# Kernel optimization log

Hardware: AMD Instinct MI355X
Metric: run time of the kernel (lower is better)

Reference implementation:

```python
import jax, jax.numpy as jnp
import numpy as np

NUM_ENTITIES = 100000
NUM_RELATIONS = 500
DIM = 256
NUM_TRIANGLES = 300000
NUM_TETRAS = 150000
ET_EDGES = 900000   # ~3 entities per triangle
TT_EDGES = 600000   # ~4 triangles per tetra
ENT_TET_EDGES = 600000
BATCH = 8192


def _mean_aggregate(src_idx, dst_idx, src, num_dst):
    """Scatter-mean of src[src_idx] into num_dst buckets keyed by dst_idx."""
    agg = jax.ops.segment_sum(src[src_idx], dst_idx, num_segments=num_dst)
    cnt = jax.ops.segment_sum(jnp.ones_like(dst_idx, dtype=src.dtype), dst_idx,
                              num_segments=num_dst)
    return agg / jnp.maximum(cnt, 1.0)[:, None]


def setup_inputs() -> dict:
    key = jax.random.key(0)
    ks = jax.random.split(key, 16)
    s = 1.0 / np.sqrt(DIM)
    E = jax.random.normal(ks[0], (NUM_ENTITIES, DIM), jnp.float32) * s
    R = jax.random.normal(ks[1], (NUM_RELATIONS, DIM), jnp.float32) * s
    lin2_w = jax.random.normal(ks[2], (DIM, DIM), jnp.float32) * s
    lin2_b = jnp.zeros((DIM,), jnp.float32)
    lin3_w = jax.random.normal(ks[3], (DIM, DIM), jnp.float32) * s
    lin3_b = jnp.zeros((DIM,), jnp.float32)
    t2e_w = jax.random.normal(ks[4], (DIM, DIM), jnp.float32) * s
    t2e_b = jnp.zeros((DIM,), jnp.float32)
    fusion_alpha = jnp.zeros((2,), jnp.float32)
    gamma = jnp.array([12.0], jnp.float32)
    # bipartite edge lists: row 0 = src indices, row 1 = dst indices
    et = jnp.stack([
        jax.random.randint(ks[5], (ET_EDGES,), 0, NUM_ENTITIES),
        jax.random.randint(ks[6], (ET_EDGES,), 0, NUM_TRIANGLES)], axis=0)
    tt = jnp.stack([
        jax.random.randint(ks[7], (TT_EDGES,), 0, NUM_TRIANGLES),
        jax.random.randint(ks[8], (TT_EDGES,), 0, NUM_TETRAS)], axis=0)
    # entity_tetra_index: row 0 = entity, row 1 = tetra (flipped inside model)
    etet = jnp.stack([
        jax.random.randint(ks[9], (ENT_TET_EDGES,), 0, NUM_ENTITIES),
        jax.random.randint(ks[10], (ENT_TET_EDGES,), 0, NUM_TETRAS)], axis=0)
    triples = jnp.stack([
        jax.random.randint(ks[11], (BATCH,), 0, NUM_ENTITIES),
        jax.random.randint(ks[12], (BATCH,), 0, NUM_RELATIONS),
        jax.random.randint(ks[13], (BATCH,), 0, NUM_ENTITIES)], axis=1)
    return {"E": E, "R": R, "lin2_w": lin2_w, "lin2_b": lin2_b,
            "lin3_w": lin3_w, "lin3_b": lin3_b, "t2e_w": t2e_w, "t2e_b": t2e_b,
            "fusion_alpha": fusion_alpha, "gamma": gamma,
            "entity_triangle_index": et, "triangle_tetra_index": tt,
            "entity_tetra_index": etet, "triples": triples,
            "num_triangles": NUM_TRIANGLES, "num_tetras": NUM_TETRAS}


def reference(E, R, lin2_w, lin2_b, lin3_w, lin3_b, t2e_w, t2e_b,
              fusion_alpha, gamma, entity_triangle_index, triangle_tetra_index,
              entity_tetra_index, triples, num_triangles, num_tetras):
    # gnn2: entity -> triangle (scatter-mean + Linear + ReLU)
    tri_agg = _mean_aggregate(entity_triangle_index[0], entity_triangle_index[1],
                              E, num_triangles)                      # [T, d]
    tri_emb = jax.nn.relu(tri_agg @ lin2_w.T + lin2_b)
    # gnn3: triangle -> tetra
    tet_agg = _mean_aggregate(triangle_tetra_index[0], triangle_tetra_index[1],
                              tri_emb, num_tetras)                   # [K, d]
    tet_emb = jax.nn.relu(tet_agg @ lin3_w.T + lin3_b)
    tet_proj = tet_emb @ t2e_w.T + t2e_b                             # [K, d]
    # tetra -> entity (edge index flipped: src=tetra, dst=entity)
    v_topo = _mean_aggregate(entity_tetra_index[1], entity_tetra_index[0],
                             tet_proj, E.shape[0])                   # [N, d]
    # learned fusion
    w = jax.nn.softmax(fusion_alpha)
    V = w[0] * E + w[1] * v_topo
    # TransE scoring: gamma - ||V[h] + R[r] - V[t]||
    h, r, t = triples[:, 0], triples[:, 1], triples[:, 2]
    diff = V[h] + R[r] - V[t]
    return gamma[0] - jnp.sqrt(jnp.sum(diff * diff, axis=-1))
```

## Files before the change

### kernel.cpp

```cpp
#include <hip/hip_runtime.h>
#include <hip/hip_bf16.h>
#include <math.h>

#define DIM 256
#define SBS 256
#define SIT 16
#define NT   300000
#define NTET 150000

typedef __attribute__((ext_vector_type(8))) short          bf16x8;
typedef __attribute__((ext_vector_type(8))) unsigned short u16x8;
typedef __attribute__((ext_vector_type(4))) float          f32x4;

__device__ inline float b2f(unsigned short u) {
    union { unsigned int i; float f; } c; c.i = ((unsigned int)u) << 16; return c.f;
}
__device__ inline unsigned short f2b(float f) {
    __hip_bfloat16 h = __float2bfloat16(f);
    return *reinterpret_cast<unsigned short*>(&h);
}
__device__ inline short f2bs(float f) { return (short)f2b(f); }
__device__ inline bool bmget(const unsigned* bm, int i) {
    return (bm[i >> 5] >> (i & 31)) & 1u;
}
__device__ inline void gll16(const void* g, void* l) {
    __builtin_amdgcn_global_load_lds(
        (const __attribute__((address_space(1))) unsigned int*)g,
        (__attribute__((address_space(3))) unsigned int*)l, 16, 0, 0);
}

__global__ __launch_bounds__(256) void k_cast3(
    const float* __restrict__ w2, const float* __restrict__ w3,
    const float* __restrict__ wt, unsigned short* __restrict__ out)
{
    int i = (blockIdx.x * 256 + threadIdx.x) * 4;
    const float* src; int l;
    if (i < 65536)       { src = w2; l = i; }
    else if (i < 131072) { src = w3; l = i - 65536; }
    else                 { src = wt; l = i - 131072; }
    float4 v = *(const float4*)(src + l);
    ushort4 o; o.x = f2b(v.x); o.y = f2b(v.y); o.z = f2b(v.z); o.w = f2b(v.w);
    *(ushort4*)(out + i) = o;
}

__global__ __launch_bounds__(256) void k_mark(
    const int* __restrict__ trip, unsigned* __restrict__ bm, int B)
{
    int i = blockIdx.x * 256 + threadIdx.x;
    if (i < 2 * B) {
        int ent = trip[(i >> 1) * 3 + ((i & 1) ? 2 : 0)];
        atomicOr(&bm[ent >> 5], 1u << (ent & 31));
    }
}

__global__ __launch_bounds__(256) void k_markf(
    const int* __restrict__ mi, const int* __restrict__ ci,
    const unsigned* __restrict__ bmIn, unsigned* __restrict__ bmOut, int n)
{
    int e = blockIdx.x * 256 + threadIdx.x;
    if (e < n && bmget(bmIn, ci[e])) {
        int m = mi[e];
        unsigned msk = 1u << (m & 31);
        if (!(bmOut[m >> 5] & msk)) atomicOr(&bmOut[m >> 5], msk);
    }
}

__global__ __launch_bounds__(256) void k_bits(
    const unsigned* __restrict__ bm, int* __restrict__ out, int n)
{
    int i = blockIdx.x * 256 + threadIdx.x;
    if (i < n) out[i] = (bm[i >> 5] >> (i & 31)) & 1u;
}

__global__ __launch_bounds__(256) void k_count_all(
    const int* __restrict__ et, const int* __restrict__ tt, const int* __restrict__ etet,
    const unsigned* __restrict__ bmTri, const unsigned* __restrict__ bmTet,
    const unsigned* __restrict__ bmEnt, int* __restrict__ cnt,
    int ET, int TT, int ETET)
{
    int e = blockIdx.x * 256 + threadIdx.x;
    if (e < ET) {
        int d = et[ET + e];
        if (bmget(bmTri, d)) atomicAdd(&cnt[d], 1);
    } else if (e < ET + TT) {
        int i = e - ET;
        int d = tt[TT + i];
        if (bmget(bmTet, d)) atomicAdd(&cnt[NT + d], 1);
    } else if (e < ET + TT + ETET) {
        int i = e - ET - TT;
        int d = etet[i];
        if (bmget(bmEnt, d)) atomicAdd(&cnt[NT + NTET + d], 1);
    }
}

__global__ __launch_bounds__(SBS) void k_scan_block(
    const int* __restrict__ cnt, int* __restrict__ rowOff,
    int* __restrict__ blockSums, int n)
{
    __shared__ int lds[SBS];
    const int t = threadIdx.x;
    const int tbase = blockIdx.x * SBS * SIT + t * SIT;
    int v[SIT]; int tsum = 0;
    #pragma unroll
    for (int i = 0; i < SIT; ++i) {
        int idx = tbase + i;
        v[i] = (idx < n) ? cnt[idx] : 0;
        tsum += v[i];
    }
    lds[t] = tsum;
    __syncthreads();
    #pragma unroll
    for (int off = 1; off < SBS; off <<= 1) {
        int y = (t >= off) ? lds[t - off] : 0;
        __syncthreads();
        lds[t] += y;
        __syncthreads();
    }
    int incl = lds[t];
    int run = incl - tsum;
    #pragma unroll
    for (int i = 0; i < SIT; ++i) {
        int idx = tbase + i;
        if (idx < n) rowOff[idx] = run;
        run += v[i];
    }
    if (t == SBS - 1) blockSums[blockIdx.x] = incl;
}

__global__ __launch_bounds__(SBS) void k_scan_sums(int* __restrict__ bs, int nb)
{
    __shared__ int lds[SBS];
    const int t = threadIdx.x;
    int v = (t < nb) ? bs[t] : 0;
    lds[t] = v;
    __syncthreads();
    #pragma unroll
    for (int off = 1; off < SBS; off <<= 1) {
        int y = (t >= off) ? lds[t - off] : 0;
        __syncthreads();
        lds[t] += y;
        __syncthreads();
    }
    if (t < nb) {
        bs[t] = lds[t] - v;
        if (t == nb - 1) bs[nb] = lds[t];
    }
}

__global__ __launch_bounds__(256) void k_scan_add(
    int* __restrict__ rowOff, int* __restrict__ cursor,
    const int* __restrict__ bs, int n, int nb, int ncur)
{
    int i = blockIdx.x * 256 + threadIdx.x;
    if (i < n) {
        int v = rowOff[i] + bs[i / (SBS * SIT)];
        rowOff[i] = v;
        if (i < ncur) cursor[i] = v;
    }
    if (i == 0) rowOff[n] = bs[nb];
}

__global__ __launch_bounds__(256) void k_place_all(
    const int* __restrict__ et, const int* __restrict__ tt, const int* __restrict__ etet,
    const unsigned* __restrict__ bmTri, const unsigned* __restrict__ bmTet,
    const unsigned* __restrict__ bmEnt, int* __restrict__ cursor,
    int* __restrict__ sorted, int ET, int TT, int ETET)
{
    int e = blockIdx.x * 256 + threadIdx.x;
    if (e < ET) {
        int d = et[ET + e];
        if (bmget(bmTri, d)) sorted[atomicAdd(&cursor[d], 1)] = et[e];
    } else if (e < ET + TT) {
        int i = e - ET;
        int d = tt[TT + i];
        if (bmget(bmTet, d)) sorted[atomicAdd(&cursor[NT + d], 1)] = tt[i];
    } else if (e < ET + TT + ETET) {
        int i = e - ET - TT;
        int d = etet[i];
        if (bmget(bmEnt, d)) sorted[atomicAdd(&cursor[NT + NTET + d], 1)] = etet[ETET + i];
    }
}

template<int EPI>
__global__ __launch_bounds__(256) void k_gather(
    const unsigned short* __restrict__ src, const int* __restrict__ sorted,
    const int* __restrict__ rowOff, const float* __restrict__ bias,
    const float* __restrict__ E, const float* __restrict__ alpha,
    const unsigned* __restrict__ bm, const int* __restrict__ cmpOff,
    void* __restrict__ out, int ndst)
{
    const int g    = (blockIdx.x * 256 + threadIdx.x) >> 6;
    const int lane = threadIdx.x & 63;
    const int half = lane >> 5;
    const int hl   = lane & 31;
    const int d    = g * 2 + half;
    const bool need = (d < ndst) && bmget(bm, d);
    if (!__any(need)) return;
    const int cmpBase = (EPI >= 1) ? cmpOff[0] : 0;
    int e0 = 0, e1 = 0;
    if (need) { e0 = rowOff[d]; e1 = rowOff[d + 1]; }
    float acc[8] = {0.f, 0.f, 0.f, 0.f, 0.f, 0.f, 0.f, 0.f};
    for (int p = e0; p < e1; p += 4) {
        u16x8 u[4]; float gt[4];
        #pragma unroll
        for (int j = 0; j < 4; ++j) {
            int ee = p + j;
            int ec = (ee < e1) ? ee : (e1 - 1);
            int s  = sorted[ec];
            if (EPI == 2) s = cmpOff[s] - cmpBase;
            u[j]  = *(const u16x8*)(src + (size_t)s * DIM + hl * 8);
            gt[j] = (ee < e1) ? 1.0f : 0.0f;
        }
        #pragma unroll
        for (int j = 0; j < 4; ++j)
            #pragma unroll
            for (int k = 0; k < 8; ++k)
                acc[k] += gt[j] * b2f(u[j][k]);
    }
    float inv = 1.0f / fmaxf((float)(e1 - e0), 1.0f);
    #pragma unroll
    for (int k = 0; k < 8; ++k) acc[k] *= inv;
    if (EPI == 0) {
        float4 bl = *(const float4*)(bias + hl * 8);
        float4 bh = *(const float4*)(bias + hl * 8 + 4);
        float bb[8] = {bl.x, bl.y, bl.z, bl.w, bh.x, bh.y, bh.z, bh.w};
        if (need) {
            u16x8 o;
            #pragma unroll
            for (int k = 0; k < 8; ++k) o[k] = f2b(fmaxf(acc[k] + bb[k], 0.f));
            *(u16x8*)((unsigned short*)out + (size_t)d * DIM + hl * 8) = o;
        }
    } else if (EPI == 1) {
        if (need) {
            int cd = cmpOff[d] - cmpBase;
            u16x8 o;
            #pragma unroll
            for (int k = 0; k < 8; ++k) o[k] = f2b(acc[k]);
            *(u16x8*)((unsigned short*)out + (size_t)cd * DIM + hl * 8) = o;
        }
    } else {
        float a0 = alpha[0], a1v = alpha[1];
        float mx = fmaxf(a0, a1v);
        float x0 = expf(a0 - mx), x1 = expf(a1v - mx);
        float w0 = x0 / (x0 + x1), w1 = x1 / (x0 + x1);
        if (need) {
            const float* er = E + (size_t)d * DIM + hl * 8;
            float4 el = *(const float4*)er;
            float4 eh = *(const float4*)(er + 4);
            float4 o0, o1;
            o0.x = w0 * el.x + w1 * acc[0]; o0.y = w0 * el.y + w1 * acc[1];
            o0.z = w0 * el.z + w1 * acc[2]; o0.w = w0 * el.w + w1 * acc[3];
            o1.x = w0 * eh.x + w1 * acc[4]; o1.y = w0 * eh.y + w1 * acc[5];
            o1.z = w0 * eh.z + w1 * acc[6]; o1.w = w0 * eh.w + w1 * acc[7];
            float* orow = (float*)out + (size_t)d * DIM + hl * 8;
            *(float4*)orow = o0;
            *(float4*)(orow + 4) = o1;
        }
    }
}

template<bool AF32, bool RELU, bool BIAS, bool DYNM>
__global__ __launch_bounds__(256) void k_gemm_mfma(
    const void* __restrict__ Ap, const unsigned short* __restrict__ Wb,
    const float* __restrict__ bias, unsigned short* __restrict__ Cp,
    int Ms, const int* __restrict__ cmpOff)
{
    int M = Ms;
    if (DYNM) M = cmpOff[NTET] - cmpOff[0];
    const int m0 = blockIdx.x * 128;
    if (m0 >= M) return;
    __shared__ __align__(16) char smem[AF32 ? 49152 : 32768];
    char* AsB = smem;
    char* WsB = smem + (AF32 ? 32768 : 16384);
    const int tid  = threadIdx.x;
    const int n0   = blockIdx.y * 128;
    const int wid  = tid >> 6, lane = tid & 63;
    const int wr   = wid >> 1, wc = wid & 1;
    const int fr   = lane & 15;
    const int fc   = lane >> 4;
    const int gA = (tid & 15) ^ ((tid >> 4) & 15);
    const int gW = (tid & 7)  ^ ((tid >> 3) & 7);

    f32x4 acc[4][4] = {};
    for (int k0 = 0; k0 < DIM; k0 += 64) {
        __syncthreads();
        if (AF32) {
            #pragma unroll
            for (int it = 0; it < 8; ++it) {
                int r  = it * 16 + (tid >> 4);
                int gm = m0 + r; if (gm >= M) gm = M - 1;
                const float* srcp = (const float*)Ap + (size_t)gm * DIM + k0 + gA * 4;
                gll16(srcp, AsB + (size_t)(it * 256 + tid) * 16);
            }
        } else {
            #pragma unroll
            for (int it = 0; it < 4; ++it) {
                int r  = it * 32 + (tid >> 3);
                int gm = m0 + r; if (gm >= M) gm = M - 1;
                const unsigned short* srcp = (const unsigned short*)Ap + (size_t)gm * DIM + k0 + gW * 8;
                gll16(srcp, AsB + (size_t)(it * 256 + tid) * 16);
            }
        }
        #pragma unroll
        for (int it = 0; it < 4; ++it) {
            int n = it * 32 + (tid >> 3);
            const unsigned short* srcp = Wb + (size_t)(n0 + n) * DIM + k0 + gW * 8;
            gll16(srcp, WsB + (size_t)(it * 256 + tid) * 16);
        }
        __syncthreads();
        #pragma unroll
        for (int kk = 0; kk < 2; ++kk) {
            bf16x8 aF[4], bF[4];
            #pragma unroll
            for (int i = 0; i < 4; ++i) {
                int ar = wr * 64 + i * 16 + fr;
                if (AF32) {
                    int p0 = kk * 8 + fc * 2;
                    const char* rb = AsB + ar * 256;
                    float4 lo = *(const float4*)(rb + ((p0       ^ (ar & 15)) * 16));
                    float4 hi = *(const float4*)(rb + (((p0 + 1) ^ (ar & 15)) * 16));
                    bf16x8 a;
                    a[0] = f2bs(lo.x); a[1] = f2bs(lo.y); a[2] = f2bs(lo.z); a[3] = f2bs(lo.w);
                    a[4] = f2bs(hi.x); a[5] = f2bs(hi.y); a[6] = f2bs(hi.z); a[7] = f2bs(hi.w);
                    aF[i] = a;
                } else {
                    int p = kk * 4 + fc;
                    aF[i] = *(const bf16x8*)(AsB + ar * 128 + ((p ^ (ar & 7)) * 16));
                }
                int wn = wc * 64 + i * 16 + fr;
                int pw = kk * 4 + fc;
                bF[i] = *(const bf16x8*)(WsB + wn * 128 + ((pw ^ (wn & 7)) * 16));
            }
            #pragma unroll
            for (int i = 0; i < 4; ++i)
                #pragma unroll
                for (int j = 0; j < 4; ++j)
                    acc[i][j] = __builtin_amdgcn_mfma_f32_16x16x32_bf16(
                        aF[i], bF[j], acc[i][j], 0, 0, 0);
        }
    }
    const int cnb   = n0 + wc * 64 + fr;
    const int rbase = m0 + wr * 64 + fc * 4;
    #pragma unroll
    for (int j = 0; j < 4; ++j) {
        float bv = BIAS ? bias[cnb + j * 16] : 0.0f;
        #pragma unroll
        for (int i = 0; i < 4; ++i) {
            #pragma unroll
            for (int q = 0; q < 4; ++q) {
                int m = rbase + i * 16 + q;
                if (m < M) {
                    float v = acc[i][j][q] + bv;
                    if (RELU) v = fmaxf(v, 0.f);
                    Cp[(size_t)m * DIM + cnb + j * 16] = f2b(v);
                }
            }
        }
    }
}

__global__ __launch_bounds__(256) void k_score(
    const float* __restrict__ V, const float* __restrict__ R,
    const int* __restrict__ triples, const float* __restrict__ gamma,
    float* __restrict__ out, int B)
{
    int t    = (blockIdx.x * 256 + threadIdx.x) >> 6;
    int lane = threadIdx.x & 63;
    if (t >= B) return;
    int h  = triples[t * 3 + 0];
    int r  = triples[t * 3 + 1];
    int tl = triples[t * 3 + 2];
    float4 vh = *(const float4*)(V + (size_t)h  * DIM + lane * 4);
    float4 vr = *(const float4*)(R + (size_t)r  * DIM + lane * 4);
    float4 vt = *(const float4*)(V + (size_t)tl * DIM + lane * 4);
    float dx = vh.x + vr.x - vt.x;
    float dy = vh.y + vr.y - vt.y;
    float dz = vh.z + vr.z - vt.z;
    float dw = vh.w + vr.w - vt.w;
    float s = dx * dx + dy * dy + dz * dz + dw * dw;
    #pragma unroll
    for (int off = 32; off > 0; off >>= 1) s += __shfl_xor(s, off);
    if (lane == 0) out[t] = gamma[0] - sqrtf(s);
}

extern "C" void kernel_launch(void* const* d_in, const int* in_sizes, int n_in,
                              void* d_out, int out_size, void* d_ws, size_t ws_size,
                              hipStream_t stream)
{
    const float* E      = (const float*)d_in[0];
    const float* R      = (const float*)d_in[1];
    const float* lin2_w = (const float*)d_in[2];
    const float* lin2_b = (const float*)d_in[3];
    const float* lin3_w = (const float*)d_in[4];
    const float* lin3_b = (const float*)d_in[5];
    const float* t2e_w  = (const float*)d_in[6];
    const float* t2e_b  = (const float*)d_in[7];
    const float* alpha  = (const float*)d_in[8];
    const float* gamma  = (const float*)d_in[9];
    const int*   et     = (const int*)d_in[10];
    const int*   tt     = (const int*)d_in[11];
    const int*   etet   = (const int*)d_in[12];
    const int*   trip   = (const int*)d_in[13];

    const int NE    = in_sizes[0] / DIM;
    const int ET    = in_sizes[10] / 2;
    const int TT    = in_sizes[11] / 2;
    const int ETET  = in_sizes[12] / 2;
    const int B     = in_sizes[13] / 3;
    const int NTOT  = NT + NTET + NE;
    const int NTOT2 = NTOT + NTET;
    const int ETOT  = ET + TT + ETET;

    char* ws = (char*)d_ws;
    const size_t P1  = (size_t)NE * DIM * 4;
    const size_t IDX = P1 + (size_t)NT * DIM * 2;
    unsigned short* EW      = (unsigned short*)ws;
    unsigned short* tetAgg  = (unsigned short*)ws;
    float*          V       = (float*)ws;
    unsigned short* triEmb  = (unsigned short*)(ws + P1);
    unsigned short* tetEmb  = (unsigned short*)(ws + P1);
    unsigned short* tetProj = (unsigned short*)(ws + P1) + (size_t)NTET * DIM;
    size_t off = IDX;
    int* sortedAll = (int*)(ws + off); off += (size_t)ETOT * 4;
    int* rowOffAll = (int*)(ws + off); off += ((size_t)(NTOT2 + 1) * 4 + 15) & ~15ull;
    int* cursorAll = (int*)(ws + off); off += (size_t)NTOT * 4;
    int* blockSums = (int*)(ws + off); off += 1040;
    unsigned short* Wb = (unsigned short*)(ws + off); off += 3 * 131072;
    char* zbase = ws + off;
    int*      cntAll = (int*)(ws + off);      off += (size_t)NTOT2 * 4;
    unsigned* bmEnt  = (unsigned*)(ws + off); off += ((size_t)(NE   + 31) / 32) * 4;
    unsigned* bmTet  = (unsigned*)(ws + off); off += ((size_t)(NTET + 31) / 32) * 4;
    unsigned* bmTri  = (unsigned*)(ws + off); off += ((size_t)(NT   + 31) / 32) * 4;
    size_t zsize = (size_t)(ws + off - zbase);
    if (ws_size < off) return;

    unsigned short* W2b = Wb;
    unsigned short* W3b = Wb + 65536;
    unsigned short* Wtb = Wb + 131072;
    int* cmpOff = rowOffAll + NTOT;

    hipMemsetAsync(zbase, 0, zsize, stream);
    k_cast3<<<192, 256, 0, stream>>>(lin2_w, lin3_w, t2e_w, Wb);
    dim3 gE((NE + 127) / 128, 2);
    k_gemm_mfma<true, false, false, false><<<gE, 256, 0, stream>>>(
        E, W2b, nullptr, EW, NE, nullptr);

    k_mark<<<(2 * B + 255) / 256, 256, 0, stream>>>(trip, bmEnt, B);
    k_markf<<<(ETET + 255) / 256, 256, 0, stream>>>(etet + ETET, etet, bmEnt, bmTet, ETET);
    k_markf<<<(TT + 255) / 256, 256, 0, stream>>>(tt, tt + TT, bmTet, bmTri, TT);
    k_bits<<<(NTET + 255) / 256, 256, 0, stream>>>(bmTet, cntAll + NTOT, NTET);

    k_count_all<<<(ETOT + 255) / 256, 256, 0, stream>>>(
        et, tt, etet, bmTri, bmTet, bmEnt, cntAll, ET, TT, ETET);
    int nb = (NTOT2 + SBS * SIT - 1) / (SBS * SIT);
    k_scan_block<<<nb, SBS, 0, stream>>>(cntAll, rowOffAll, blockSums, NTOT2);
    k_scan_sums<<<1, SBS, 0, stream>>>(blockSums, nb);
    k_scan_add<<<(NTOT2 + 255) / 256, 256, 0, stream>>>(rowOffAll, cursorAll,
                                                        blockSums, NTOT2, nb, NTOT);
    k_place_all<<<(ETOT + 255) / 256, 256, 0, stream>>>(
        et, tt, etet, bmTri, bmTet, bmEnt, cursorAll, sortedAll, ET, TT, ETET);

    k_gather<0><<<(NT + 7) / 8, 256, 0, stream>>>(EW, sortedAll, rowOffAll, lin2_b,
                                                  nullptr, nullptr, bmTri, cmpOff,
                                                  triEmb, NT);

    k_gather<1><<<(NTET + 7) / 8, 256, 0, stream>>>(triEmb, sortedAll, rowOffAll + NT,
                                                    nullptr, nullptr, nullptr, bmTet,
                                                    cmpOff, tetAgg, NTET);
    dim3 gT((NTET + 127) / 128, 2);
    k_gemm_mfma<false, true, true, true><<<gT, 256, 0, stream>>>(
        tetAgg, W3b, lin3_b, tetEmb, NTET, cmpOff);
    k_gemm_mfma<false, false, true, true><<<gT, 256, 0, stream>>>(
        tetEmb, Wtb, t2e_b, tetProj, NTET, cmpOff);

    k_gather<2><<<(NE + 7) / 8, 256, 0, stream>>>(tetProj, sortedAll,
                                                  rowOffAll + NT + NTET, nullptr,
                                                  E, alpha, bmEnt, cmpOff, V, NE);

    k_score<<<(B + 3) / 4, 256, 0, stream>>>(V, R, trip, gamma, (float*)d_out, B);
}
```

Measured before the change: 413.4 us.

## Make GEMM keep weight slice resident in LDS with persistent row-chunk loop

Replaces the tiled 128x128 MFMA GEMM with a persistent 512-thread kernel that loads a 128-column slice of the bf16 weight matrix (full K=256) into LDS once. Each wave then streams 32-row chunks of A straight from global memory into registers and computes against the resident weights. The aim is to stop reloading W tiles per block and drop the per-k-step LDS staging and barriers for A. In exchange, A reads are no longer staged through LDS, register use is higher, and the grid is fixed at 256x2.

New measurement: 436.5 us. 1.06x slower.

```diff
diff --git a/kernel.cpp b/kernel.cpp
--- a/kernel.cpp
+++ b/kernel.cpp
@@ -260,99 +260,88 @@
 }
 
 template<bool AF32, bool RELU, bool BIAS, bool DYNM>
-__global__ __launch_bounds__(256) void k_gemm_mfma(
+__global__ __launch_bounds__(512) void k_gemm_wres(
     const void* __restrict__ Ap, const unsigned short* __restrict__ Wb,
     const float* __restrict__ bias, unsigned short* __restrict__ Cp,
     int Ms, const int* __restrict__ cmpOff)
 {
     int M = Ms;
     if (DYNM) M = cmpOff[NTET] - cmpOff[0];
-    const int m0 = blockIdx.x * 128;
-    if (m0 >= M) return;
-    __shared__ __align__(16) char smem[AF32 ? 49152 : 32768];
-    char* AsB = smem;
-    char* WsB = smem + (AF32 ? 32768 : 16384);
-    const int tid  = threadIdx.x;
-    const int n0   = blockIdx.y * 128;
-    const int wid  = tid >> 6, lane = tid & 63;
-    const int wr   = wid >> 1, wc = wid & 1;
-    const int fr   = lane & 15;
-    const int fc   = lane >> 4;
-    const int gA = (tid & 15) ^ ((tid >> 4) & 15);
-    const int gW = (tid & 7)  ^ ((tid >> 3) & 7);
-
-    f32x4 acc[4][4] = {};
-    for (int k0 = 0; k0 < DIM; k0 += 64) {
-        __syncthreads();
-        if (AF32) {
-            #pragma unroll
-            for (int it = 0; it < 8; ++it) {
-                int r  = it * 16 + (tid >> 4);
-                int gm = m0 + r; if (gm >= M) gm = M - 1;
-                const float* srcp = (const float*)Ap + (size_t)gm * DIM + k0 + gA * 4;
-                gll16(srcp, AsB + (size_t)(it * 256 + tid) * 16);
-            }
-        } else {
-            #pragma unroll
-            for (int it = 0; it < 4; ++it) {
-                int r  = it * 32 + (tid >> 3);
-                int gm = m0 + r; if (gm >= M) gm = M - 1;
-                const unsigned short* srcp = (const unsigned short*)Ap + (size_t)gm * DIM + k0 + gW * 8;
-                gll16(srcp, AsB + (size_t)(it * 256 + tid) * 16);
-            }
-        }
-        #pragma unroll
-        for (int it = 0; it < 4; ++it) {
-            int n = it * 32 + (tid >> 3);
-            const unsigned short* srcp = Wb + (size_t)(n0 + n) * DIM + k0 + gW * 8;
-            gll16(srcp, WsB + (size_t)(it * 256 + tid) * 16);
-        }
-        __syncthreads();
-        #pragma unroll
-        for (int kk = 0; kk < 2; ++kk) {
-            bf16x8 aF[4], bF[4];
-            #pragma unroll
-            for (int i = 0; i < 4; ++i) {
-                int ar = wr * 64 + i * 16 + fr;
-                if (AF32) {
-                    int p0 = kk * 8 + fc * 2;
-                    const char* rb = AsB + ar * 256;
-                    float4 lo = *(const float4*)(rb + ((p0       ^ (ar & 15)) * 16));
-                    float4 hi = *(const float4*)(rb + (((p0 + 1) ^ (ar & 15)) * 16));
+    __shared__ __align__(16) unsigned short Wl[128 * 256];
+    const int tid = threadIdx.x;
+    const int n0b = blockIdx.y * 128;
+    {
+        int s  = tid & 31;
+        int r0 = tid >> 5;
+        #pragma unroll
+        for (int it = 0; it < 8; ++it) {
+            int r  = it * 16 + r0;
+            int sp = (s & 24) | ((s & 7) ^ (r & 7));
+            const unsigned short* g = Wb + (size_t)(n0b + r) * DIM + sp * 8;
+            gll16(g, (char*)Wl + ((size_t)r * 32 + s) * 16);
+        }
+    }
+    __syncthreads();
+    if (M <= 0) return;
+    const int w    = tid >> 6, lane = tid & 63;
+    const int fr   = lane & 15, fc = lane >> 4;
+    const int nsub = w & 1, rstream = w >> 1;
+    const int n0w  = nsub * 64;
+    const int nch  = (M + 31) >> 5;
+    for (int c = blockIdx.x * 4 + rstream; c < nch; c += gridDim.x * 4) {
+        const int rbase = c * 32;
+        bf16x8 aF[2][8];
+        #pragma unroll
+        for (int rt = 0; rt < 2; ++rt) {
+            int row = rbase + rt * 16 + fr;
+            if (row >= M) row = M - 1;
+            if (AF32) {
+                const float* ar = (const float*)Ap + (size_t)row * DIM;
+                #pragma unroll
+                for (int kf = 0; kf < 8; ++kf) {
+                    float4 lo = *(const float4*)(ar + kf * 32 + fc * 8);
+                    float4 hi = *(const float4*)(ar + kf * 32 + fc * 8 + 4);
                     bf16x8 a;
                     a[0] = f2bs(lo.x); a[1] = f2bs(lo.y); a[2] = f2bs(lo.z); a[3] = f2bs(lo.w);
                     a[4] = f2bs(hi.x); a[5] = f2bs(hi.y); a[6] = f2bs(hi.z); a[7] = f2bs(hi.w);
-                    aF[i] = a;
-                } else {
-                    int p = kk * 4 + fc;
-                    aF[i] = *(const bf16x8*)(AsB + ar * 128 + ((p ^ (ar & 7)) * 16));
+                    aF[rt][kf] = a;
                 }
-                int wn = wc * 64 + i * 16 + fr;
-                int pw = kk * 4 + fc;
-                bF[i] = *(const bf16x8*)(WsB + wn * 128 + ((pw ^ (wn & 7)) * 16));
+            } else {
+                const unsigned short* ar = (const unsigned short*)Ap + (size_t)row * DIM;
+                #pragma unroll
+                for (int kf = 0; kf < 8; ++kf)
+                    aF[rt][kf] = *(const bf16x8*)(ar + kf * 32 + fc * 8);
             }
+        }
+        f32x4 acc[2][4] = {};
+        #pragma unroll
+        for (int kf = 0; kf < 8; ++kf) {
             #pragma unroll
-            for (int i = 0; i < 4; ++i)
+            for (int nf = 0; nf < 4; ++nf) {
+                int rL   = n0w + nf * 16 + fr;
+                int p    = kf * 4 + fc;
+                int slot = (p & 24) | ((p & 7) ^ (rL & 7));
+                bf16x8 bF = *(const bf16x8*)((const char*)Wl + (size_t)rL * 512 + slot * 16);
                 #pragma unroll
-                for (int j = 0; j < 4; ++j)
-                    acc[i][j] = __builtin_amdgcn_mfma_f32_16x16x32_bf16(
-                        aF[i], bF[j], acc[i][j], 0, 0, 0);
-        }
-    }
-    const int cnb   = n0 + wc * 64 + fr;
-    const int rbase = m0 + wr * 64 + fc * 4;
-    #pragma unroll
-    for (int j = 0; j < 4; ++j) {
-        float bv = BIAS ? bias[cnb + j * 16] : 0.0f;
-        #pragma unroll
-        for (int i = 0; i < 4; ++i) {
+                for (int rt = 0; rt < 2; ++rt)
+                    acc[rt][nf] = __builtin_amdgcn_mfma_f32_16x16x32_bf16(
+                        aF[rt][kf], bF, acc[rt][nf], 0, 0, 0);
+            }
+        }
+        #pragma unroll
+        for (int nf = 0; nf < 4; ++nf) {
+            int col = n0b + n0w + nf * 16 + fr;
+            float bv = BIAS ? bias[col] : 0.0f;
             #pragma unroll
-            for (int q = 0; q < 4; ++q) {
-                int m = rbase + i * 16 + q;
-                if (m < M) {
-                    float v = acc[i][j][q] + bv;
-                    if (RELU) v = fmaxf(v, 0.f);
-                    Cp[(size_t)m * DIM + cnb + j * 16] = f2b(v);
+            for (int rt = 0; rt < 2; ++rt) {
+                #pragma unroll
+                for (int q = 0; q < 4; ++q) {
+                    int m = rbase + rt * 16 + fc * 4 + q;
+                    if (m < M) {
+                        float v = acc[rt][nf][q] + bv;
+                        if (RELU) v = fmaxf(v, 0.f);
+                        Cp[(size_t)m * DIM + col] = f2b(v);
+                    }
                 }
             }
         }
@@ -441,8 +430,8 @@
 
     hipMemsetAsync(zbase, 0, zsize, stream);
     k_cast3<<<192, 256, 0, stream>>>(lin2_w, lin3_w, t2e_w, Wb);
-    dim3 gE((NE + 127) / 128, 2);
-    k_gemm_mfma<true, false, false, false><<<gE, 256, 0, stream>>>(
+    dim3 gW(256, 2);
+    k_gemm_wres<true, false, false, false><<<gW, 512, 0, stream>>>(
         E, W2b, nullptr, EW, NE, nullptr);
 
     k_mark<<<(2 * B + 255) / 256, 256, 0, stream>>>(trip, bmEnt, B);
@@ -467,10 +456,9 @@
     k_gather<1><<<(NTET + 7) / 8, 256, 0, stream>>>(triEmb, sortedAll, rowOffAll + NT,
                                                     nullptr, nullptr, nullptr, bmTet,
                                                     cmpOff, tetAgg, NTET);
-    dim3 gT((NTET + 127) / 128, 2);
-    k_gemm_mfma<false, true, true, true><<<gT, 256, 0, stream>>>(
+    k_gemm_wres<false, true, true, true><<<gW, 512, 0, stream>>>(
         tetAgg, W3b, lin3_b, tetEmb, NTET, cmpOff);
-    k_gemm_mfma<false, false, true, true><<<gT, 256, 0, stream>>>(
+    k_gemm_wres<false, false, true, true><<<gW, 512, 0, stream>>>(
         tetEmb, Wtb, t2e_b, tetProj, NTET, cmpOff);
 
     k_gather<2><<<(NE + 7) / 8, 256, 0, stream>>>(tetProj, sortedAll,
```

## Double-buffer GEMM LDS tiles with K-step 32 to overlap loads and MFMA

Applied to the files above, without the earlier changes.

The MFMA GEMM kernel now uses two LDS buffers with a K-step of 32 instead of a single buffer with a K-step of 64. The next tile is prefetched while MFMAs run on the current one, and the swizzle patterns are adjusted to the narrower rows. This aims to hide global-to-LDS load latency behind compute and removes one barrier per iteration. The cost is twice as many iterations, each with a barrier, and a possible LDS bank-conflict change from the new swizzle.

New measurement: 424.3 us. 1.03x slower.

```diff
diff --git a/kernel.cpp b/kernel.cpp
--- a/kernel.cpp
+++ b/kernel.cpp
@@ -269,67 +269,78 @@
     if (DYNM) M = cmpOff[NTET] - cmpOff[0];
     const int m0 = blockIdx.x * 128;
     if (m0 >= M) return;
-    __shared__ __align__(16) char smem[AF32 ? 49152 : 32768];
-    char* AsB = smem;
-    char* WsB = smem + (AF32 ? 32768 : 16384);
+    constexpr int ABYTES = AF32 ? 16384 : 8192;
+    constexpr int BUF    = ABYTES + 8192;
+    __shared__ __align__(16) char smem[2 * BUF];
     const int tid  = threadIdx.x;
     const int n0   = blockIdx.y * 128;
     const int wid  = tid >> 6, lane = tid & 63;
     const int wr   = wid >> 1, wc = wid & 1;
     const int fr   = lane & 15;
     const int fc   = lane >> 4;
-    const int gA = (tid & 15) ^ ((tid >> 4) & 15);
-    const int gW = (tid & 7)  ^ ((tid >> 3) & 7);
-
-    f32x4 acc[4][4] = {};
-    for (int k0 = 0; k0 < DIM; k0 += 64) {
-        __syncthreads();
+
+    auto stage = [&](int buf, int k0) {
+        char* AsB = smem + buf * BUF;
+        char* WsB = AsB + ABYTES;
         if (AF32) {
             #pragma unroll
-            for (int it = 0; it < 8; ++it) {
-                int r  = it * 16 + (tid >> 4);
+            for (int it = 0; it < 4; ++it) {
+                int q = it * 256 + tid;
+                int r = q >> 3, s = q & 7;
                 int gm = m0 + r; if (gm >= M) gm = M - 1;
-                const float* srcp = (const float*)Ap + (size_t)gm * DIM + k0 + gA * 4;
-                gll16(srcp, AsB + (size_t)(it * 256 + tid) * 16);
+                int sp = s ^ (r & 7);
+                gll16((const float*)Ap + (size_t)gm * DIM + k0 + sp * 4,
+                      AsB + (size_t)q * 16);
             }
         } else {
             #pragma unroll
-            for (int it = 0; it < 4; ++it) {
-                int r  = it * 32 + (tid >> 3);
+            for (int it = 0; it < 2; ++it) {
+                int q = it * 256 + tid;
+                int r = q >> 2, s = q & 3;
                 int gm = m0 + r; if (gm >= M) gm = M - 1;
-                const unsigned short* srcp = (const unsigned short*)Ap + (size_t)gm * DIM + k0 + gW * 8;
-                gll16(srcp, AsB + (size_t)(it * 256 + tid) * 16);
+                int sp = s ^ ((r >> 1) & 3);
+                gll16((const unsigned short*)Ap + (size_t)gm * DIM + k0 + sp * 8,
+                      AsB + (size_t)q * 16);
             }
         }
         #pragma unroll
-        for (int it = 0; it < 4; ++it) {
-            int n = it * 32 + (tid >> 3);
-            const unsigned short* srcp = Wb + (size_t)(n0 + n) * DIM + k0 + gW * 8;
-            gll16(srcp, WsB + (size_t)(it * 256 + tid) * 16);
-        }
-        __syncthreads();
-        #pragma unroll
-        for (int kk = 0; kk < 2; ++kk) {
+        for (int it = 0; it < 2; ++it) {
+            int q = it * 256 + tid;
+            int r = q >> 2, s = q & 3;
+            int sp = s ^ ((r >> 1) & 3);
+            gll16(Wb + (size_t)(n0 + r) * DIM + k0 + sp * 8,
+                  WsB + (size_t)q * 16);
+        }
+    };
+
+    f32x4 acc[4][4] = {};
+    stage(0, 0);
+    __syncthreads();
+    int cur = 0;
+    #pragma unroll
+    for (int st = 0; st < 8; ++st) {
+        if (st < 7) stage(cur ^ 1, (st + 1) * 32);
+        {
+            char* AsB = smem + cur * BUF;
+            char* WsB = AsB + ABYTES;
             bf16x8 aF[4], bF[4];
             #pragma unroll
             for (int i = 0; i < 4; ++i) {
                 int ar = wr * 64 + i * 16 + fr;
                 if (AF32) {
-                    int p0 = kk * 8 + fc * 2;
-                    const char* rb = AsB + ar * 256;
-                    float4 lo = *(const float4*)(rb + ((p0       ^ (ar & 15)) * 16));
-                    float4 hi = *(const float4*)(rb + (((p0 + 1) ^ (ar & 15)) * 16));
+                    const char* rb = AsB + ar * 128;
+                    int p0 = fc * 2;
+                    float4 lo = *(const float4*)(rb + ((p0       ^ (ar & 7)) * 16));
+                    float4 hi = *(const float4*)(rb + (((p0 + 1) ^ (ar & 7)) * 16));
                     bf16x8 a;
                     a[0] = f2bs(lo.x); a[1] = f2bs(lo.y); a[2] = f2bs(lo.z); a[3] = f2bs(lo.w);
                     a[4] = f2bs(hi.x); a[5] = f2bs(hi.y); a[6] = f2bs(hi.z); a[7] = f2bs(hi.w);
                     aF[i] = a;
                 } else {
-                    int p = kk * 4 + fc;
-                    aF[i] = *(const bf16x8*)(AsB + ar * 128 + ((p ^ (ar & 7)) * 16));
+                    aF[i] = *(const bf16x8*)(AsB + ar * 64 + ((fc ^ ((ar >> 1) & 3)) * 16));
                 }
                 int wn = wc * 64 + i * 16 + fr;
-                int pw = kk * 4 + fc;
-                bF[i] = *(const bf16x8*)(WsB + wn * 128 + ((pw ^ (wn & 7)) * 16));
+                bF[i] = *(const bf16x8*)(WsB + wn * 64 + ((fc ^ ((wn >> 1) & 3)) * 16));
             }
             #pragma unroll
             for (int i = 0; i < 4; ++i)
@@ -338,6 +349,8 @@
                     acc[i][j] = __builtin_amdgcn_mfma_f32_16x16x32_bf16(
                         aF[i], bF[j], acc[i][j], 0, 0, 0);
         }
+        __syncthreads();
+        cur ^= 1;
     }
     const int cnb   = n0 + wc * 64 + fr;
     const int rbase = m0 + wr * 64 + fc * 4;
```
